# Optimization experiments

Hardware: AMD Instinct MI355X
Metric: run time of the kernel (lower is better)

Reference implementation:

```python
import jax, jax.numpy as jnp
import numpy as np

EPS = 1e-5

def _layernorm(x, g, b):
    mu = jnp.mean(x, axis=-1, keepdims=True)
    var = jnp.mean(jnp.square(x - mu), axis=-1, keepdims=True)
    return (x - mu) * jax.lax.rsqrt(var + EPS) * g + b

def setup_inputs() -> dict:
    key = jax.random.key(0)
    ks = jax.random.split(key, 6)
    B, S, D = 4, 2048, 1024
    F = 4 * D
    return {
        "hidden_states": jax.random.normal(ks[0], (B, S, D), jnp.float32),
        "w_qkv": jax.random.normal(ks[1], (D, 3 * D), jnp.float32) * (D ** -0.5),
        "fc1_w": jax.random.normal(ks[2], (D, F), jnp.float32) * (D ** -0.5),
        "fc1_b": jax.random.normal(ks[3], (F,), jnp.float32) * 0.02,
        "fc2_w": jax.random.normal(ks[4], (F, D), jnp.float32) * (F ** -0.5),
        "fc2_b": jax.random.normal(ks[5], (D,), jnp.float32) * 0.02,
        "ln1_g": jnp.ones((D,), jnp.float32),
        "ln1_b": jnp.zeros((D,), jnp.float32),
        "ln2_g": jnp.ones((D,), jnp.float32),
        "ln2_b": jnp.zeros((D,), jnp.float32),
    }

def reference(hidden_states, w_qkv, fc1_w, fc1_b, fc2_w, fc2_b, ln1_g, ln1_b, ln2_g, ln2_b):
    D = hidden_states.shape[-1]
    residual = hidden_states
    h = _layernorm(hidden_states, ln1_g, ln1_b)
    qkv = jnp.einsum('bsd,de->bse', h, w_qkv)  # [B,S,3D]
    q, k, v = jnp.split(qkv, 3, axis=-1)
    # single-head attention, NO 1/sqrt(d) scaling, no mask (faithful to source)
    scores = jnp.einsum('bsd,btd->bst', q, k)  # [B,S,S]
    w = jax.nn.softmax(scores, axis=-1)
    attn = jnp.einsum('bst,btd->bsd', w, v)
    h = attn + residual
    residual = h
    h = _layernorm(h, ln2_g, ln2_b)
    h = jnp.einsum('bsd,df->bsf', h, fc1_w) + fc1_b
    h = jax.nn.gelu(h, approximate=False)  # torch nn.GELU default is exact erf
    h = jnp.einsum('bsf,fd->bsd', h, fc2_w) + fc2_b
    return h + residual
```

## Files before the change

### kernel.cpp

```cpp
#include <hip/hip_runtime.h>
#include <math.h>

typedef unsigned short u16;
typedef unsigned int u32;
typedef _Float16 f16x8 __attribute__((ext_vector_type(8)));
typedef float f32x4 __attribute__((ext_vector_type(4)));
typedef u16 u16x4 __attribute__((ext_vector_type(4)));

__device__ __forceinline__ u16 f2h(float x) {
  _Float16 h = (_Float16)x;
  return __builtin_bit_cast(u16, h);
}
__device__ __forceinline__ float h2f(u16 u) {
  return (float)__builtin_bit_cast(_Float16, u);
}

__device__ __forceinline__ void gload16(const void* g, void* l) {
  __builtin_amdgcn_global_load_lds(
      (const __attribute__((address_space(1))) void*)g,
      (__attribute__((address_space(3))) void*)l, 16, 0, 0);
}

template <int JF, int NPH, int EPI, bool SWZ>
__global__ __launch_bounds__(512, 2) void gemm8(
    const u16* __restrict__ A, const u16* __restrict__ B, int M, int N, int K,
    int lda, int ldb, long zsA, long zsB, long zsC, float* __restrict__ outF,
    u16* __restrict__ outU, const float* __restrict__ aux0,
    const float* __restrict__ aux1) {
  constexpr int BUF = 32768 + JF * 8192;
  constexpr int IPP = 8 / NPH;
  extern __shared__ __align__(16) char smem[];

  const int tid = threadIdx.x;
  const int lane = tid & 63;
  const int wave = tid >> 6;
  const int z = blockIdx.z;

  int bx = blockIdx.x, by = blockIdx.y;
  if constexpr (SWZ) {
    const int gx = gridDim.x;
    const int nwg = gx * gridDim.y;
    const int id = by * gx + bx;
    const int q = nwg >> 3;
    const int id2 = (id & 7) * q + (id >> 3);
    bx = id2 % gx;
    by = id2 / gx;
  }
  const long row0 = (long)by * 256;
  const long col0 = (long)bx * (64 * JF);

  const u16* __restrict__ Ab = A + (long)z * zsA;
  const u16* __restrict__ Bb = B + (long)z * zsB;

  const int srow = lane >> 3;
  const int gslot = (lane & 7) ^ srow;
  const int fr = lane & 15;
  const int kgrp = lane >> 4;
  const int wm = (wave >> 2) << 7;
  const int wn = (wave & 3) * (16 * JF);

  const int nk = K >> 6;

  const int slot0 = kgrp ^ (fr & 7);
  const int offA0 = (wm + fr) * 128 + slot0 * 16;
  const int offA1 = offA0 ^ 64;
  const int offB0 = 32768 + (wn + fr) * 128 + slot0 * 16;
  const int offB1 = offB0 ^ 64;

  const u16* const gA0 = Ab + (row0 + wave * 16 + srow) * (long)lda + gslot * 8;
  const u16* const gA1 = gA0 + 128 * (long)lda;
  const u16* const gB0 = Bb + (col0 + wave * 16 + srow) * (long)ldb + gslot * 8;
  const u16* const gB1 = gB0 + 128 * (long)ldb;
  char* const dA = smem + wave * 2048 + lane * 16;
  char* const dB = dA + 32768;

  f32x4 acc[8][JF] = {};
  f16x8 bfrag[2][JF];

  auto stageA = [&](int buf, int kt, int h) {
    const long ko = (long)kt * 64;
    const u16* g = (h ? gA1 : gA0) + ko;
    char* d = dA + buf * BUF + (h ? 16384 : 0);
    gload16(g, d);
    gload16(g + 8 * (long)lda, d + 1024);
  };
  auto stageB = [&](int buf, int kt, int h) {
    const long ko = (long)kt * 64;
    const u16* g = (h ? gB1 : gB0) + ko;
    char* d = dB + buf * BUF + (h ? 16384 : 0);
    gload16(g, d);
    gload16(g + 8 * (long)ldb, d + 1024);
  };

  stageA(0, 0, 0);
  stageA(0, 0, 1);
  stageB(0, 0, 0);
  if constexpr (JF == 4) stageB(0, 0, 1);
  stageB(1, 1, 0);
  if constexpr (JF == 4) stageB(1, 1, 1);
  if constexpr (JF == 4)
    asm volatile("s_waitcnt vmcnt(4)");
  else
    asm volatile("s_waitcnt vmcnt(2)");
  __builtin_amdgcn_s_barrier();

  for (int s = 0; s < nk; ++s) {
    const int cur = s & 1;
    const bool stA = (s + 1 < nk);
    const bool stB = (s + 2 < nk);
    const char* sb = smem + cur * BUF;
    const char* pA0 = sb + offA0;
    const char* pA1 = sb + offA1;
    const char* pB0 = sb + offB0;
    const char* pB1 = sb + offB1;
#pragma unroll
    for (int p = 0; p < NPH; ++p) {
      f16x8 af[IPP][2];
#pragma unroll
      for (int ii = 0; ii < IPP; ++ii) {
        af[ii][0] = *(const f16x8*)(pA0 + (p * IPP + ii) * 2048);
        af[ii][1] = *(const f16x8*)(pA1 + (p * IPP + ii) * 2048);
      }
      if (p == 0) {
#pragma unroll
        for (int j = 0; j < JF; ++j) {
          bfrag[0][j] = *(const f16x8*)(pB0 + j * 2048);
          bfrag[1][j] = *(const f16x8*)(pB1 + j * 2048);
        }
      }
      if (p == 0 && stA) stageA(cur ^ 1, s + 1, 0);
      if (p == 1) {
        if (stA) stageA(cur ^ 1, s + 1, 1);
        if (stB) stageB(cur, s + 2, 0);
      }
      if constexpr (NPH == 4) {
        if (p == 2 && stB) stageB(cur, s + 2, 1);
      }
      __builtin_amdgcn_s_barrier();
      asm volatile("s_waitcnt lgkmcnt(0)");
      __builtin_amdgcn_s_setprio(1);
#pragma unroll
      for (int kk = 0; kk < 2; ++kk)
#pragma unroll
        for (int ii = 0; ii < IPP; ++ii)
#pragma unroll
          for (int j = 0; j < JF; ++j)
            acc[p * IPP + ii][j] = __builtin_amdgcn_mfma_f32_16x16x32_f16(
                af[ii][kk], bfrag[kk][j], acc[p * IPP + ii][j], 0, 0, 0);
      __builtin_amdgcn_s_setprio(0);
      if (p == NPH - 1) {
        if (stB) {
          if constexpr (JF == 4)
            asm volatile("s_waitcnt vmcnt(4)");
          else
            asm volatile("s_waitcnt vmcnt(2)");
        } else {
          asm volatile("s_waitcnt vmcnt(0)");
        }
      }
      __builtin_amdgcn_s_barrier();
    }
  }

#pragma unroll
  for (int i = 0; i < 8; ++i) {
#pragma unroll
    for (int j = 0; j < JF; ++j) {
#pragma unroll
      for (int r = 0; r < 4; ++r) {
        const long m = row0 + wm + i * 16 + (kgrp << 2) + r;
        const long n = col0 + wn + j * 16 + fr;
        const float val = acc[i][j][r];
        if constexpr (EPI == 1) {
          outF[(long)z * zsC + m * (long)N + n] = val;
        } else if constexpr (EPI == 2) {
          const long idx = (long)z * zsC + m * (long)N + n;
          outF[idx] = val + aux0[idx];
        } else if constexpr (EPI == 3) {
          const float t = val + aux0[n];
          const float gl = 0.5f * t * (1.0f + erff(t * 0.70710678118654752f));
          outU[m * (long)N + n] = f2h(gl);
        } else if constexpr (EPI == 4) {
          outF[m * (long)N + n] = val + aux0[n] + aux1[m * (long)N + n];
        } else {
          outU[m * (long)N + n] = f2h(val);
        }
      }
    }
  }
}

__global__ __launch_bounds__(256) void ln_k(const float* __restrict__ x,
                                            const float* __restrict__ gw,
                                            const float* __restrict__ bw,
                                            u16* __restrict__ out) {
  const int lane = threadIdx.x & 63;
  const int wv = threadIdx.x >> 6;
  const long row = (long)blockIdx.x * 4 + wv;
  const float* xr = x + row * 1024;
  float4 v[4];
  float s = 0.f, ss = 0.f;
#pragma unroll
  for (int j = 0; j < 4; ++j) {
    v[j] = *(const float4*)(xr + (lane + 64 * j) * 4);
    s += v[j].x + v[j].y + v[j].z + v[j].w;
    ss += v[j].x * v[j].x + v[j].y * v[j].y + v[j].z * v[j].z + v[j].w * v[j].w;
  }
#pragma unroll
  for (int o = 32; o; o >>= 1) {
    s += __shfl_xor(s, o);
    ss += __shfl_xor(ss, o);
  }
  const float mu = s * (1.f / 1024.f);
  const float var = ss * (1.f / 1024.f) - mu * mu;
  const float rs = rsqrtf(var + 1e-5f);
  u16* orow = out + row * 1024;
#pragma unroll
  for (int j = 0; j < 4; ++j) {
    const int n = (lane + 64 * j) * 4;
    const float4 gg = *(const float4*)(gw + n);
    const float4 bb = *(const float4*)(bw + n);
    u16x4 H;
    H[0] = f2h((v[j].x - mu) * rs * gg.x + bb.x);
    H[1] = f2h((v[j].y - mu) * rs * gg.y + bb.y);
    H[2] = f2h((v[j].z - mu) * rs * gg.z + bb.z);
    H[3] = f2h((v[j].w - mu) * rs * gg.w + bb.w);
    *(u16x4*)(orow + n) = H;
  }
}

template <int MODE>
__global__ __launch_bounds__(256) void transpose_k(const void* __restrict__ in,
                                                   u16* __restrict__ out,
                                                   int R, int C, long zsIn,
                                                   long zsOut) {
  __shared__ float tile[32][33];
  const int z = blockIdx.z;
  const int c0 = blockIdx.x * 32, r0 = blockIdx.y * 32;
#pragma unroll
  for (int i = 0; i < 4; ++i) {
    const int lin = threadIdx.x + 256 * i;
    const int rr = lin >> 5, cc = lin & 31;
    float vv;
    if constexpr (MODE == 2)
      vv = h2f(((const u16*)in + (long)z * zsIn)[(long)(r0 + rr) * C + c0 + cc]);
    else
      vv = ((const float*)in)[(long)(r0 + rr) * C + c0 + cc];
    tile[rr][cc] = vv;
  }
  __syncthreads();
  u16* outz = out + (long)z * zsOut;
#pragma unroll
  for (int i = 0; i < 4; ++i) {
    const int lin = threadIdx.x + 256 * i;
    const int oc = lin >> 5, orr = lin & 31;
    outz[(long)(c0 + oc) * R + (r0 + orr)] = f2h(tile[orr][oc]);
  }
}

__global__ __launch_bounds__(256) void softmax_k(float* __restrict__ S) {
  const long row = blockIdx.x;
  float* sr = S + row * 2048;
  u16* pr = (u16*)sr;
  const int tid = threadIdx.x;
  const int lane = tid & 63, wv = tid >> 6;
  __shared__ float red[8];
  const float4 v0 = *(const float4*)(sr + tid * 4);
  const float4 v1 = *(const float4*)(sr + 1024 + tid * 4);
  float mx = fmaxf(fmaxf(fmaxf(v0.x, v0.y), fmaxf(v0.z, v0.w)),
                   fmaxf(fmaxf(v1.x, v1.y), fmaxf(v1.z, v1.w)));
#pragma unroll
  for (int o = 32; o; o >>= 1) mx = fmaxf(mx, __shfl_xor(mx, o));
  if (lane == 0) red[wv] = mx;
  __syncthreads();
  mx = fmaxf(fmaxf(red[0], red[1]), fmaxf(red[2], red[3]));
  float e[8];
  e[0] = expf(v0.x - mx); e[1] = expf(v0.y - mx);
  e[2] = expf(v0.z - mx); e[3] = expf(v0.w - mx);
  e[4] = expf(v1.x - mx); e[5] = expf(v1.y - mx);
  e[6] = expf(v1.z - mx); e[7] = expf(v1.w - mx);
  float sm = e[0] + e[1] + e[2] + e[3] + e[4] + e[5] + e[6] + e[7];
#pragma unroll
  for (int o = 32; o; o >>= 1) sm += __shfl_xor(sm, o);
  if (lane == 0) red[4 + wv] = sm;
  __syncthreads();
  sm = red[4] + red[5] + red[6] + red[7];
  const float inv = 1.f / sm;
  u16x4 a, b;
  a[0] = f2h(e[0] * inv); a[1] = f2h(e[1] * inv);
  a[2] = f2h(e[2] * inv); a[3] = f2h(e[3] * inv);
  b[0] = f2h(e[4] * inv); b[1] = f2h(e[5] * inv);
  b[2] = f2h(e[6] * inv); b[3] = f2h(e[7] * inv);
  *(u16x4*)(pr + tid * 4) = a;
  *(u16x4*)(pr + 1024 + tid * 4) = b;
}

extern "C" void kernel_launch(void* const* d_in, const int* in_sizes, int n_in,
                              void* d_out, int out_size, void* d_ws,
                              size_t ws_size, hipStream_t stream) {
  const float* x     = (const float*)d_in[0];
  const float* w_qkv = (const float*)d_in[1];
  const float* fc1_w = (const float*)d_in[2];
  const float* fc1_b = (const float*)d_in[3];
  const float* fc2_w = (const float*)d_in[4];
  const float* fc2_b = (const float*)d_in[5];
  const float* ln1_g = (const float*)d_in[6];
  const float* ln1_b = (const float*)d_in[7];
  const float* ln2_g = (const float*)d_in[8];
  const float* ln2_b = (const float*)d_in[9];
  float* out = (float*)d_out;

  char* ws = (char*)d_ws;
  const long MB = 1024L * 1024L;
  u16*   h    = (u16*)(ws + 0);
  u16*   wqkT = (u16*)(ws + 16 * MB);
  float* sc   = (float*)(ws + 0);
  u16*   qk   = (u16*)(ws + 64 * MB);
  u16*   vbuf = (u16*)(ws + 96 * MB);
  u16*   vT   = (u16*)(ws + 112 * MB);
  u16*   w1T  = (u16*)(ws + 144 * MB);
  u16*   w2T  = (u16*)(ws + 152 * MB);
  float* r2   = (float*)(ws + 64 * MB);
  u16*   h2   = (u16*)(ws + 96 * MB);
  u16*   g    = (u16*)(ws + 0);

  dim3 blk(256);
  dim3 blk8(512);
  const int LDS4 = 131072;
  const int LDS2 = 98304;
  (void)hipFuncSetAttribute((const void*)gemm8<4, 4, 5, true>,
                            hipFuncAttributeMaxDynamicSharedMemorySize, LDS4);
  (void)hipFuncSetAttribute((const void*)gemm8<2, 2, 5, true>,
                            hipFuncAttributeMaxDynamicSharedMemorySize, LDS2);
  (void)hipFuncSetAttribute((const void*)gemm8<4, 4, 1, true>,
                            hipFuncAttributeMaxDynamicSharedMemorySize, LDS4);
  (void)hipFuncSetAttribute((const void*)gemm8<2, 2, 2, true>,
                            hipFuncAttributeMaxDynamicSharedMemorySize, LDS2);
  (void)hipFuncSetAttribute((const void*)gemm8<4, 4, 3, true>,
                            hipFuncAttributeMaxDynamicSharedMemorySize, LDS4);
  (void)hipFuncSetAttribute((const void*)gemm8<2, 2, 4, true>,
                            hipFuncAttributeMaxDynamicSharedMemorySize, LDS2);

  ln_k<<<2048, blk, 0, stream>>>(x, ln1_g, ln1_b, h);
  transpose_k<0><<<dim3(3072 / 32, 1024 / 32, 1), blk, 0, stream>>>(
      w_qkv, wqkT, 1024, 3072, 0, 0);
  gemm8<4, 4, 5, true><<<dim3(8, 32, 1), blk8, LDS4, stream>>>(
      h, wqkT, 8192, 2048, 1024, 1024, 1024, 0, 0, 0, nullptr, qk, nullptr,
      nullptr);
  gemm8<2, 2, 5, true><<<dim3(8, 32, 1), blk8, LDS2, stream>>>(
      h, wqkT + 2048L * 1024, 8192, 1024, 1024, 1024, 1024, 0, 0, 0, nullptr,
      vbuf, nullptr, nullptr);
  transpose_k<2><<<dim3(1024 / 32, 2048 / 32, 4), blk, 0, stream>>>(
      vbuf, vT, 2048, 1024, 2048L * 1024, 1024L * 2048);
  gemm8<4, 4, 1, true><<<dim3(8, 8, 4), blk8, LDS4, stream>>>(
      qk, qk + 1024, 2048, 2048, 1024, 2048, 2048, 2048L * 2048, 2048L * 2048,
      2048L * 2048, sc, nullptr, nullptr, nullptr);
  softmax_k<<<8192, blk, 0, stream>>>(sc);
  gemm8<2, 2, 2, true><<<dim3(8, 8, 4), blk8, LDS2, stream>>>(
      (const u16*)sc, vT, 2048, 1024, 2048, 4096, 2048, 2048L * 4096,
      1024L * 2048, 2048L * 1024, r2, nullptr, x, nullptr);
  ln_k<<<2048, blk, 0, stream>>>(r2, ln2_g, ln2_b, h2);
  transpose_k<0><<<dim3(4096 / 32, 1024 / 32, 1), blk, 0, stream>>>(
      fc1_w, w1T, 1024, 4096, 0, 0);
  transpose_k<0><<<dim3(1024 / 32, 4096 / 32, 1), blk, 0, stream>>>(
      fc2_w, w2T, 4096, 1024, 0, 0);
  gemm8<4, 4, 3, true><<<dim3(16, 32, 1), blk8, LDS4, stream>>>(
      h2, w1T, 8192, 4096, 1024, 1024, 1024, 0, 0, 0, nullptr, g, fc1_b,
      nullptr);
  gemm8<2, 2, 4, true><<<dim3(8, 32, 1), blk8, LDS2, stream>>>(
      g, w2T, 8192, 1024, 4096, 4096, 4096, 0, 0, 0, out, nullptr, fc2_b, r2);
}
```

Baseline: 404.9 us.

## Replace pipelined 256-row GEMM with simple single-buffered 128x128 tile GEMM

Replaces the 512-thread, double-buffered, phase-interleaved GEMM (256xJF*64 tiles, dynamic LDS up to 128KB) with a 256-thread kernel that computes 128x128 tiles from a single 32KB static LDS buffer. Global loads are synchronous with __syncthreads around each K step. The Q/K and V projections are merged into one launch whose epilogue splits the output columns. This gives more, smaller blocks and higher occupancy, at the cost of losing load/compute overlap and tile reuse per block.

```diff
diff --git a/kernel.cpp b/kernel.cpp
--- a/kernel.cpp
+++ b/kernel.cpp
@@ -21,15 +21,15 @@
       (__attribute__((address_space(3))) void*)l, 16, 0, 0);
 }
 
-template <int JF, int NPH, int EPI, bool SWZ>
-__global__ __launch_bounds__(512, 2) void gemm8(
+template <int EPI, bool SWZ>
+__global__ __launch_bounds__(256, 2) void gemm_nt(
     const u16* __restrict__ A, const u16* __restrict__ B, int M, int N, int K,
     int lda, int ldb, long zsA, long zsB, long zsC, float* __restrict__ outF,
-    u16* __restrict__ outU, const float* __restrict__ aux0,
-    const float* __restrict__ aux1) {
-  constexpr int BUF = 32768 + JF * 8192;
-  constexpr int IPP = 8 / NPH;
-  extern __shared__ __align__(16) char smem[];
+    u16* __restrict__ outU, u16* __restrict__ outU2,
+    const float* __restrict__ aux0, const float* __restrict__ aux1) {
+  __shared__ char smem[2 * 128 * 64 * 2];
+  char* sA = smem;
+  char* sB = smem + 16384;
 
   const int tid = threadIdx.x;
   const int lane = tid & 63;
@@ -46,132 +46,79 @@
     bx = id2 % gx;
     by = id2 / gx;
   }
-  const long row0 = (long)by * 256;
-  const long col0 = (long)bx * (64 * JF);
+  const long row0 = (long)by * 128;
+  const long col0 = (long)bx * 128;
 
   const u16* __restrict__ Ab = A + (long)z * zsA;
   const u16* __restrict__ Bb = B + (long)z * zsB;
 
   const int srow = lane >> 3;
-  const int gslot = (lane & 7) ^ srow;
+  const int sslot = (lane & 7) ^ srow;
+
+  const int wm = (wave >> 1) << 6;
+  const int wn = (wave & 1) << 6;
   const int fr = lane & 15;
   const int kgrp = lane >> 4;
-  const int wm = (wave >> 2) << 7;
-  const int wn = (wave & 3) * (16 * JF);
-
+
+  f32x4 acc[4][4] = {};
   const int nk = K >> 6;
 
-  const int slot0 = kgrp ^ (fr & 7);
-  const int offA0 = (wm + fr) * 128 + slot0 * 16;
-  const int offA1 = offA0 ^ 64;
-  const int offB0 = 32768 + (wn + fr) * 128 + slot0 * 16;
-  const int offB1 = offB0 ^ 64;
-
-  const u16* const gA0 = Ab + (row0 + wave * 16 + srow) * (long)lda + gslot * 8;
-  const u16* const gA1 = gA0 + 128 * (long)lda;
-  const u16* const gB0 = Bb + (col0 + wave * 16 + srow) * (long)ldb + gslot * 8;
-  const u16* const gB1 = gB0 + 128 * (long)ldb;
-  char* const dA = smem + wave * 2048 + lane * 16;
-  char* const dB = dA + 32768;
-
-  f32x4 acc[8][JF] = {};
-  f16x8 bfrag[2][JF];
-
-  auto stageA = [&](int buf, int kt, int h) {
-    const long ko = (long)kt * 64;
-    const u16* g = (h ? gA1 : gA0) + ko;
-    char* d = dA + buf * BUF + (h ? 16384 : 0);
-    gload16(g, d);
-    gload16(g + 8 * (long)lda, d + 1024);
+  auto stage = [&](int kt) {
+#pragma unroll
+    for (int c = 0; c < 4; ++c) {
+      const int chunk = wave * 4 + c;
+      const int r = chunk * 8 + srow;
+      gload16(Ab + (row0 + r) * (long)lda + kt * 64 + sslot * 8,
+              sA + chunk * 1024);
+      gload16(Bb + (col0 + r) * (long)ldb + kt * 64 + sslot * 8,
+              sB + chunk * 1024);
+    }
   };
-  auto stageB = [&](int buf, int kt, int h) {
-    const long ko = (long)kt * 64;
-    const u16* g = (h ? gB1 : gB0) + ko;
-    char* d = dB + buf * BUF + (h ? 16384 : 0);
-    gload16(g, d);
-    gload16(g + 8 * (long)ldb, d + 1024);
-  };
-
-  stageA(0, 0, 0);
-  stageA(0, 0, 1);
-  stageB(0, 0, 0);
-  if constexpr (JF == 4) stageB(0, 0, 1);
-  stageB(1, 1, 0);
-  if constexpr (JF == 4) stageB(1, 1, 1);
-  if constexpr (JF == 4)
-    asm volatile("s_waitcnt vmcnt(4)");
-  else
-    asm volatile("s_waitcnt vmcnt(2)");
-  __builtin_amdgcn_s_barrier();
-
-  for (int s = 0; s < nk; ++s) {
-    const int cur = s & 1;
-    const bool stA = (s + 1 < nk);
-    const bool stB = (s + 2 < nk);
-    const char* sb = smem + cur * BUF;
-    const char* pA0 = sb + offA0;
-    const char* pA1 = sb + offA1;
-    const char* pB0 = sb + offB0;
-    const char* pB1 = sb + offB1;
-#pragma unroll
-    for (int p = 0; p < NPH; ++p) {
-      f16x8 af[IPP][2];
-#pragma unroll
-      for (int ii = 0; ii < IPP; ++ii) {
-        af[ii][0] = *(const f16x8*)(pA0 + (p * IPP + ii) * 2048);
-        af[ii][1] = *(const f16x8*)(pA1 + (p * IPP + ii) * 2048);
+
+  stage(0);
+  for (int kt = 0; kt < nk; ++kt) {
+    __syncthreads();
+#pragma unroll
+    for (int kk = 0; kk < 2; ++kk) {
+      f16x8 af[4], bg[4];
+#pragma unroll
+      for (int i = 0; i < 4; ++i) {
+        const int r = wm + i * 16 + fr;
+        const int slot = ((kk << 2) | kgrp) ^ (r & 7);
+        af[i] = *(const f16x8*)(sA + r * 128 + slot * 16);
       }
-      if (p == 0) {
-#pragma unroll
-        for (int j = 0; j < JF; ++j) {
-          bfrag[0][j] = *(const f16x8*)(pB0 + j * 2048);
-          bfrag[1][j] = *(const f16x8*)(pB1 + j * 2048);
-        }
+#pragma unroll
+      for (int j = 0; j < 4; ++j) {
+        const int r = wn + j * 16 + fr;
+        const int slot = ((kk << 2) | kgrp) ^ (r & 7);
+        bg[j] = *(const f16x8*)(sB + r * 128 + slot * 16);
       }
-      if (p == 0 && stA) stageA(cur ^ 1, s + 1, 0);
-      if (p == 1) {
-        if (stA) stageA(cur ^ 1, s + 1, 1);
-        if (stB) stageB(cur, s + 2, 0);
-      }
-      if constexpr (NPH == 4) {
-        if (p == 2 && stB) stageB(cur, s + 2, 1);
-      }
-      __builtin_amdgcn_s_barrier();
-      asm volatile("s_waitcnt lgkmcnt(0)");
-      __builtin_amdgcn_s_setprio(1);
-#pragma unroll
-      for (int kk = 0; kk < 2; ++kk)
-#pragma unroll
-        for (int ii = 0; ii < IPP; ++ii)
-#pragma unroll
-          for (int j = 0; j < JF; ++j)
-            acc[p * IPP + ii][j] = __builtin_amdgcn_mfma_f32_16x16x32_f16(
-                af[ii][kk], bfrag[kk][j], acc[p * IPP + ii][j], 0, 0, 0);
-      __builtin_amdgcn_s_setprio(0);
-      if (p == NPH - 1) {
-        if (stB) {
-          if constexpr (JF == 4)
-            asm volatile("s_waitcnt vmcnt(4)");
-          else
-            asm volatile("s_waitcnt vmcnt(2)");
-        } else {
-          asm volatile("s_waitcnt vmcnt(0)");
-        }
-      }
-      __builtin_amdgcn_s_barrier();
+#pragma unroll
+      for (int i = 0; i < 4; ++i)
+#pragma unroll
+        for (int j = 0; j < 4; ++j)
+          acc[i][j] = __builtin_amdgcn_mfma_f32_16x16x32_f16(af[i], bg[j],
+                                                             acc[i][j], 0, 0, 0);
     }
-  }
-
-#pragma unroll
-  for (int i = 0; i < 8; ++i) {
-#pragma unroll
-    for (int j = 0; j < JF; ++j) {
+    __syncthreads();
+    if (kt + 1 < nk) stage(kt + 1);
+  }
+
+#pragma unroll
+  for (int i = 0; i < 4; ++i) {
+#pragma unroll
+    for (int j = 0; j < 4; ++j) {
 #pragma unroll
       for (int r = 0; r < 4; ++r) {
         const long m = row0 + wm + i * 16 + (kgrp << 2) + r;
         const long n = col0 + wn + j * 16 + fr;
         const float val = acc[i][j][r];
-        if constexpr (EPI == 1) {
+        if constexpr (EPI == 0) {
+          if (n < 2048)
+            outU[m * 2048 + n] = f2h(val);
+          else
+            outU2[m * 1024 + (n - 2048)] = f2h(val);
+        } else if constexpr (EPI == 1) {
           outF[(long)z * zsC + m * (long)N + n] = val;
         } else if constexpr (EPI == 2) {
           const long idx = (long)z * zsC + m * (long)N + n;
@@ -180,10 +127,8 @@
           const float t = val + aux0[n];
           const float gl = 0.5f * t * (1.0f + erff(t * 0.70710678118654752f));
           outU[m * (long)N + n] = f2h(gl);
-        } else if constexpr (EPI == 4) {
+        } else {
           outF[m * (long)N + n] = val + aux0[n] + aux1[m * (long)N + n];
-        } else {
-          outU[m * (long)N + n] = f2h(val);
         }
       }
     }
@@ -325,48 +270,31 @@
   u16*   g    = (u16*)(ws + 0);
 
   dim3 blk(256);
-  dim3 blk8(512);
-  const int LDS4 = 131072;
-  const int LDS2 = 98304;
-  (void)hipFuncSetAttribute((const void*)gemm8<4, 4, 5, true>,
-                            hipFuncAttributeMaxDynamicSharedMemorySize, LDS4);
-  (void)hipFuncSetAttribute((const void*)gemm8<2, 2, 5, true>,
-                            hipFuncAttributeMaxDynamicSharedMemorySize, LDS2);
-  (void)hipFuncSetAttribute((const void*)gemm8<4, 4, 1, true>,
-                            hipFuncAttributeMaxDynamicSharedMemorySize, LDS4);
-  (void)hipFuncSetAttribute((const void*)gemm8<2, 2, 2, true>,
-                            hipFuncAttributeMaxDynamicSharedMemorySize, LDS2);
-  (void)hipFuncSetAttribute((const void*)gemm8<4, 4, 3, true>,
-                            hipFuncAttributeMaxDynamicSharedMemorySize, LDS4);
-  (void)hipFuncSetAttribute((const void*)gemm8<2, 2, 4, true>,
-                            hipFuncAttributeMaxDynamicSharedMemorySize, LDS2);
 
   ln_k<<<2048, blk, 0, stream>>>(x, ln1_g, ln1_b, h);
   transpose_k<0><<<dim3(3072 / 32, 1024 / 32, 1), blk, 0, stream>>>(
       w_qkv, wqkT, 1024, 3072, 0, 0);
-  gemm8<4, 4, 5, true><<<dim3(8, 32, 1), blk8, LDS4, stream>>>(
-      h, wqkT, 8192, 2048, 1024, 1024, 1024, 0, 0, 0, nullptr, qk, nullptr,
-      nullptr);
-  gemm8<2, 2, 5, true><<<dim3(8, 32, 1), blk8, LDS2, stream>>>(
-      h, wqkT + 2048L * 1024, 8192, 1024, 1024, 1024, 1024, 0, 0, 0, nullptr,
-      vbuf, nullptr, nullptr);
+  gemm_nt<0, true><<<dim3(24, 64, 1), blk, 0, stream>>>(
+      h, wqkT, 8192, 3072, 1024, 1024, 1024, 0, 0, 0, nullptr, qk, vbuf,
+      nullptr, nullptr);
   transpose_k<2><<<dim3(1024 / 32, 2048 / 32, 4), blk, 0, stream>>>(
       vbuf, vT, 2048, 1024, 2048L * 1024, 1024L * 2048);
-  gemm8<4, 4, 1, true><<<dim3(8, 8, 4), blk8, LDS4, stream>>>(
+  gemm_nt<1, true><<<dim3(16, 16, 4), blk, 0, stream>>>(
       qk, qk + 1024, 2048, 2048, 1024, 2048, 2048, 2048L * 2048, 2048L * 2048,
-      2048L * 2048, sc, nullptr, nullptr, nullptr);
+      2048L * 2048, sc, nullptr, nullptr, nullptr, nullptr);
   softmax_k<<<8192, blk, 0, stream>>>(sc);
-  gemm8<2, 2, 2, true><<<dim3(8, 8, 4), blk8, LDS2, stream>>>(
+  gemm_nt<2, true><<<dim3(8, 16, 4), blk, 0, stream>>>(
       (const u16*)sc, vT, 2048, 1024, 2048, 4096, 2048, 2048L * 4096,
-      1024L * 2048, 2048L * 1024, r2, nullptr, x, nullptr);
+      1024L * 2048, 2048L * 1024, r2, nullptr, nullptr, x, nullptr);
   ln_k<<<2048, blk, 0, stream>>>(r2, ln2_g, ln2_b, h2);
   transpose_k<0><<<dim3(4096 / 32, 1024 / 32, 1), blk, 0, stream>>>(
       fc1_w, w1T, 1024, 4096, 0, 0);
   transpose_k<0><<<dim3(1024 / 32, 4096 / 32, 1), blk, 0, stream>>>(
       fc2_w, w2T, 4096, 1024, 0, 0);
-  gemm8<4, 4, 3, true><<<dim3(16, 32, 1), blk8, LDS4, stream>>>(
-      h2, w1T, 8192, 4096, 1024, 1024, 1024, 0, 0, 0, nullptr, g, fc1_b,
-      nullptr);
-  gemm8<2, 2, 4, true><<<dim3(8, 32, 1), blk8, LDS2, stream>>>(
-      g, w2T, 8192, 1024, 4096, 4096, 4096, 0, 0, 0, out, nullptr, fc2_b, r2);
-}
+  gemm_nt<3, true><<<dim3(32, 64, 1), blk, 0, stream>>>(
+      h2, w1T, 8192, 4096, 1024, 1024, 1024, 0, 0, 0, nullptr, g, nullptr,
+      fc1_b, nullptr);
+  gemm_nt<4, true><<<dim3(8, 64, 1), blk, 0, stream>>>(
+      g, w2T, 8192, 1024, 4096, 4096, 4096, 0, 0, 0, out, nullptr, nullptr,
+      fc2_b, r2);
+}
```

Result: faster. 377.3 us (-6.8%).
